# Optimization experiments

Measured on AMD Instinct MI355X. Metric: run time of the kernel, lower is better.

## Reference

```python
import jax, jax.numpy as jnp
import numpy as np

EMBED = 1024
HEADS = 16
HEAD_DIM = EMBED // HEADS
SCALE = HEAD_DIM ** -0.5


def setup_inputs() -> dict:
    key = jax.random.key(0)
    ks = jax.random.split(key, 5)
    B, N = 2, 2048
    x = jax.random.normal(ks[0], (B, N, EMBED), dtype=jnp.float32)
    # qkv Linear: weight [3*EMBED, EMBED], bias [3*EMBED]
    w_qkv = jax.random.normal(ks[1], (3 * EMBED, EMBED), dtype=jnp.float32) * (EMBED ** -0.5)
    b_qkv = jnp.zeros((3 * EMBED,), dtype=jnp.float32)
    # proj Linear: weight [EMBED, EMBED], bias [EMBED]
    w_proj = jax.random.normal(ks[2], (EMBED, EMBED), dtype=jnp.float32) * (EMBED ** -0.5)
    b_proj = jnp.zeros((EMBED,), dtype=jnp.float32)
    return {"x": x, "w_qkv": w_qkv, "b_qkv": b_qkv, "w_proj": w_proj, "b_proj": b_proj}


def reference(x, w_qkv, b_qkv, w_proj, b_proj):
    B, N, _ = x.shape
    # QKV projection: [B, N, 3*EMBED]
    qkv = jnp.einsum('bnc,dc->bnd', x, w_qkv) + b_qkv
    qkv = qkv.reshape(B, N, 3, HEADS, HEAD_DIM).transpose(2, 0, 3, 1, 4)  # [3, B, H, N, Dh]
    q, k, v = qkv[0], qkv[1], qkv[2]
    # Explicit attention: matmul -> scale -> softmax -> matmul (eval mode, no dropout)
    attn = jnp.einsum('bhqd,bhkd->bhqk', q, k) * SCALE
    attn = jax.nn.softmax(attn, axis=-1)
    out = jnp.einsum('bhqk,bhkd->bhqd', attn, v)
    out = out.transpose(0, 2, 1, 3).reshape(B, N, EMBED)
    # Output projection (gamma1 is Identity; dropouts are zero in eval)
    out = jnp.einsum('bnc,dc->bnd', out, w_proj) + b_proj
    return out
```

## Files before the change

kernel.cpp:

```cpp
#include <hip/hip_runtime.h>
#include <stdint.h>

#define SEQ 2048

typedef __attribute__((ext_vector_type(8))) short bf16x8;
typedef __attribute__((ext_vector_type(4))) float f32x4;
typedef __attribute__((ext_vector_type(4))) int i32x4;

typedef const __attribute__((address_space(1))) unsigned int GVT;
typedef __attribute__((address_space(3))) unsigned int LVT;

static __device__ __forceinline__ unsigned short f2bf(float f) {
  unsigned u = __builtin_bit_cast(unsigned, f);
  u += 0x7fffu + ((u >> 16) & 1u);
  return (unsigned short)(u >> 16);
}

static __device__ __forceinline__ unsigned pk_bf16(float lo, float hi) {
  unsigned r;
  asm("v_cvt_pk_bf16_f32 %0, %1, %2" : "=v"(r) : "v"(lo), "v"(hi));
  return r;
}

__global__ __launch_bounds__(256) void cvt3_kernel(
    const float* __restrict__ s0, unsigned short* __restrict__ d0, int n0,
    const float* __restrict__ s1, unsigned short* __restrict__ d1, int n1,
    const float* __restrict__ s2, unsigned short* __restrict__ d2, int n2) {
  int i = blockIdx.x * 256 + threadIdx.x;
  const int stride = gridDim.x * 256;
  const int total = n0 + n1 + n2;
  for (; i < total; i += stride) {
    const float* s;
    unsigned short* d;
    int k;
    if (i < n0) { s = s0; d = d0; k = i; }
    else if (i < n0 + n1) { s = s1; d = d1; k = i - n0; }
    else { s = s2; d = d2; k = i - n0 - n1; }
    float4 v = reinterpret_cast<const float4*>(s)[k];
    ushort4 o;
    o.x = f2bf(v.x); o.y = f2bf(v.y); o.z = f2bf(v.z); o.w = f2bf(v.w);
    reinterpret_cast<ushort4*>(d)[k] = o;
  }
}

__global__ __launch_bounds__(256, 3) void gemm_qkv_kernel(
    const unsigned short* __restrict__ A,
    const unsigned short* __restrict__ Bt,
    const float* __restrict__ bias,
    unsigned short* __restrict__ qb,
    unsigned short* __restrict__ kbuf,
    unsigned short* __restrict__ vtbuf) {
  __shared__ __align__(16) unsigned short As[2][128 * 32];
  __shared__ __align__(16) unsigned short Bs[2][128 * 32];
  const int tid = threadIdx.x;
  const int lane = tid & 63;
  const int wid = tid >> 6;
  const int wr = wid >> 1, wc = wid & 1;
  const int lin = blockIdx.y * 24 + blockIdx.x;
  const int wg = (lin & 7) * 96 + (lin >> 3);
  const int bm = wg / 24, bn = wg % 24;
  const int lr = lane & 15, hg = lane >> 4;

  f32x4 acc[4][4] = {};

  const int r0 = tid >> 2;
  const int c0 = (tid & 3) * 8;

  auto STAGE = [&](int b, int kt) {
    const unsigned short* ga0 = A + (size_t)(bm * 128 + r0) * 1024 + kt * 32 + c0;
    const unsigned short* ga1 = A + (size_t)(bm * 128 + r0 + 64) * 1024 + kt * 32 + c0;
    const unsigned short* gb0 = Bt + (size_t)(bn * 128 + r0) * 1024 + kt * 32 + c0;
    const unsigned short* gb1 = Bt + (size_t)(bn * 128 + r0 + 64) * 1024 + kt * 32 + c0;
    __builtin_amdgcn_global_load_lds((GVT*)ga0, (LVT*)&As[b][tid * 8], 16, 0, 0);
    __builtin_amdgcn_global_load_lds((GVT*)ga1, (LVT*)&As[b][(tid + 256) * 8], 16, 0, 0);
    __builtin_amdgcn_global_load_lds((GVT*)gb0, (LVT*)&Bs[b][tid * 8], 16, 0, 0);
    __builtin_amdgcn_global_load_lds((GVT*)gb1, (LVT*)&Bs[b][(tid + 256) * 8], 16, 0, 0);
  };

  STAGE(0, 0);
  int cur = 0;
  for (int kt = 0; kt < 32; ++kt) {
    __syncthreads();
    if (kt + 1 < 32) STAGE(cur ^ 1, kt + 1);
    bf16x8 af[4], bfr[4];
#pragma unroll
    for (int i = 0; i < 4; ++i) {
      af[i] = *reinterpret_cast<const bf16x8*>(&As[cur][(wr * 64 + i * 16 + lr) * 32 + hg * 8]);
      bfr[i] = *reinterpret_cast<const bf16x8*>(&Bs[cur][(wc * 64 + i * 16 + lr) * 32 + hg * 8]);
    }
    __builtin_amdgcn_s_setprio(1);
#pragma unroll
    for (int i = 0; i < 4; ++i)
#pragma unroll
      for (int j = 0; j < 4; ++j)
        acc[i][j] = __builtin_amdgcn_mfma_f32_16x16x32_bf16(af[i], bfr[j], acc[i][j], 0, 0, 0);
    __builtin_amdgcn_s_setprio(0);
    cur ^= 1;
  }

#pragma unroll
  for (int j = 0; j < 4; ++j) {
    const int col = bn * 128 + wc * 64 + j * 16 + lr;
    const float bv = bias[col];
    const int which = col >> 10;
    const int hh = (col >> 6) & 15;
    const int dh = col & 63;
    const float scl = which == 0 ? 0.18033688011112042f : 1.0f;
#pragma unroll
    for (int i = 0; i < 4; ++i) {
      if (which == 2) {
        const int row0 = bm * 128 + wr * 64 + i * 16 + hg * 4;
        const int b = row0 >> 11, n0 = row0 & 2047;
        ushort4 vv;
        vv.x = f2bf(acc[i][j][0] + bv);
        vv.y = f2bf(acc[i][j][1] + bv);
        vv.z = f2bf(acc[i][j][2] + bv);
        vv.w = f2bf(acc[i][j][3] + bv);
        *reinterpret_cast<ushort4*>(
            &vtbuf[((size_t)((b * 16 + hh) * 64 + dh)) * 2048 + n0]) = vv;
      } else {
        unsigned short* dst = which == 0 ? qb : kbuf;
#pragma unroll
        for (int r = 0; r < 4; ++r) {
          const int row = bm * 128 + wr * 64 + i * 16 + hg * 4 + r;
          const int b = row >> 11, n = row & 2047;
          dst[((size_t)((b * 16 + hh) * 2048 + n)) * 64 + dh] = f2bf((acc[i][j][r] + bv) * scl);
        }
      }
    }
  }
}

__global__ __launch_bounds__(256, 2) void gemm_proj_kernel(
    const unsigned short* __restrict__ A,
    const unsigned short* __restrict__ Bt,
    const float* __restrict__ bias,
    float* __restrict__ out) {
  __shared__ __align__(16) unsigned short As[2][64 * 32];
  __shared__ __align__(16) unsigned short Bs[2][128 * 32];
  const int tid = threadIdx.x;
  const int lane = tid & 63;
  const int wc = tid >> 6;
  const int lin = blockIdx.y * 8 + blockIdx.x;
  const int wg = (lin & 7) * 64 + (lin >> 3);
  const int bm = wg >> 3, bn = wg & 7;
  const int lr = lane & 15, hg = lane >> 4;

  f32x4 acc[4][2] = {};
  const int r0 = tid >> 2;
  const int c0 = (tid & 3) * 8;

  auto STAGE = [&](int b, int kt) {
    const unsigned short* ga0 = A + (size_t)(bm * 64 + r0) * 1024 + kt * 32 + c0;
    const unsigned short* gb0 = Bt + (size_t)(bn * 128 + r0) * 1024 + kt * 32 + c0;
    const unsigned short* gb1 = Bt + (size_t)(bn * 128 + r0 + 64) * 1024 + kt * 32 + c0;
    __builtin_amdgcn_global_load_lds((GVT*)ga0, (LVT*)&As[b][tid * 8], 16, 0, 0);
    __builtin_amdgcn_global_load_lds((GVT*)gb0, (LVT*)&Bs[b][tid * 8], 16, 0, 0);
    __builtin_amdgcn_global_load_lds((GVT*)gb1, (LVT*)&Bs[b][(tid + 256) * 8], 16, 0, 0);
  };

  STAGE(0, 0);
  int cur = 0;
  for (int kt = 0; kt < 32; ++kt) {
    __syncthreads();
    if (kt + 1 < 32) STAGE(cur ^ 1, kt + 1);
    bf16x8 af[4], bfr[2];
#pragma unroll
    for (int i = 0; i < 4; ++i)
      af[i] = *reinterpret_cast<const bf16x8*>(&As[cur][(i * 16 + lr) * 32 + hg * 8]);
#pragma unroll
    for (int j = 0; j < 2; ++j)
      bfr[j] = *reinterpret_cast<const bf16x8*>(&Bs[cur][(wc * 32 + j * 16 + lr) * 32 + hg * 8]);
    __builtin_amdgcn_s_setprio(1);
#pragma unroll
    for (int i = 0; i < 4; ++i)
#pragma unroll
      for (int j = 0; j < 2; ++j)
        acc[i][j] = __builtin_amdgcn_mfma_f32_16x16x32_bf16(af[i], bfr[j], acc[i][j], 0, 0, 0);
    __builtin_amdgcn_s_setprio(0);
    cur ^= 1;
  }

#pragma unroll
  for (int j = 0; j < 2; ++j) {
    const int col = bn * 128 + wc * 32 + j * 16 + lr;
    const float bv = bias[col];
#pragma unroll
    for (int i = 0; i < 4; ++i)
#pragma unroll
      for (int r = 0; r < 4; ++r) {
        const int row = bm * 64 + i * 16 + hg * 4 + r;
        out[(size_t)row * 1024 + col] = acc[i][j][r] + bv;
      }
  }
}

__global__ __launch_bounds__(512, 4) void attn_kernel(
    const unsigned short* __restrict__ qb,
    const unsigned short* __restrict__ kbuf,
    const unsigned short* __restrict__ vt,
    unsigned short* __restrict__ ao) {
  __shared__ __align__(16) unsigned short KVbuf[2][2][2][4096];
  const int tid = threadIdx.x;
  const int lane = tid & 63;
  const int wid = tid >> 6;
  const int ws = wid >> 2;
  const int wq = wid & 3;
  const int lr = lane & 15;
  const int hg = lane >> 4;
  const int lin = blockIdx.y * 16 + blockIdx.x;
  const int wg = (lin & 7) * 64 + (lin >> 3);
  const int qt = wg & 15;
  const int bh = wg >> 4;
  const size_t hbase = (size_t)bh * SEQ * 64;

  bf16x8 qf[2][2];
#pragma unroll
  for (int m = 0; m < 2; ++m) {
    const unsigned short* qp =
        qb + hbase + (size_t)(qt * 128 + wq * 32 + m * 16 + lr) * 64 + hg * 8;
    qf[m][0] = *reinterpret_cast<const bf16x8*>(qp);
    qf[m][1] = *reinterpret_cast<const bf16x8*>(qp + 32);
  }

  f32x4 accO[2][4] = {};
  float l_run[2] = {0.0f, 0.0f};

  const int srow = tid >> 3;
  const int ssw = ((tid & 7) ^ (srow & 7)) * 8;
  auto STAGE = [&](int b, int kt) {
#pragma unroll
    for (int s = 0; s < 2; ++s) {
      const unsigned short* gk =
          kbuf + hbase + (size_t)(s * 1024 + kt * 64 + srow) * 64 + ssw;
      __builtin_amdgcn_global_load_lds((GVT*)gk, (LVT*)&KVbuf[0][s][b][tid * 8], 16, 0, 0);
      const unsigned short* gv =
          vt + hbase + (size_t)srow * 2048 + s * 1024 + kt * 64 + ssw;
      __builtin_amdgcn_global_load_lds((GVT*)gv, (LVT*)&KVbuf[1][s][b][tid * 8], 16, 0, 0);
    }
  };

  STAGE(0, 0);
  int cur = 0;
  const int sw0 = (hg ^ (lr & 7)) * 8;
  const int sw1 = ((hg + 4) ^ (lr & 7)) * 8;

  for (int kt = 0; kt < 16; ++kt) {
    __syncthreads();
    if (kt + 1 < 16) STAGE(cur ^ 1, kt + 1);

    const unsigned short* Ksb = &KVbuf[0][ws][cur][0];
    const unsigned short* Vsb = &KVbuf[1][ws][cur][0];

    f32x4 accT[2][4] = {};
    __builtin_amdgcn_s_setprio(1);
#pragma unroll
    for (int j = 0; j < 4; ++j) {
      const bf16x8 kf0 = *reinterpret_cast<const bf16x8*>(&Ksb[(j * 16 + lr) * 64 + sw0]);
      const bf16x8 kf1 = *reinterpret_cast<const bf16x8*>(&Ksb[(j * 16 + lr) * 64 + sw1]);
      accT[0][j] = __builtin_amdgcn_mfma_f32_16x16x32_bf16(kf0, qf[0][0], accT[0][j], 0, 0, 0);
      accT[0][j] = __builtin_amdgcn_mfma_f32_16x16x32_bf16(kf1, qf[0][1], accT[0][j], 0, 0, 0);
      accT[1][j] = __builtin_amdgcn_mfma_f32_16x16x32_bf16(kf0, qf[1][0], accT[1][j], 0, 0, 0);
      accT[1][j] = __builtin_amdgcn_mfma_f32_16x16x32_bf16(kf1, qf[1][1], accT[1][j], 0, 0, 0);
    }
    __builtin_amdgcn_s_setprio(0);

    bf16x8 pB[2][2];
#pragma unroll
    for (int m = 0; m < 2; ++m) {
      unsigned w[4][2];
      float ps0 = 0.f, ps1 = 0.f;
#pragma unroll
      for (int j = 0; j < 4; ++j) {
        const float p0 = __builtin_amdgcn_exp2f(accT[m][j][0]);
        const float p1 = __builtin_amdgcn_exp2f(accT[m][j][1]);
        const float p2 = __builtin_amdgcn_exp2f(accT[m][j][2]);
        const float p3 = __builtin_amdgcn_exp2f(accT[m][j][3]);
        ps0 += (p0 + p1);
        ps1 += (p2 + p3);
        w[j][0] = pk_bf16(p0, p1);
        w[j][1] = pk_bf16(p2, p3);
      }
      l_run[m] += ps0 + ps1;
#pragma unroll
      for (int h = 0; h < 2; ++h) {
        unsigned e0 = w[2 * h][0], e1 = w[2 * h][1];
        unsigned f0 = w[2 * h + 1][0], f1 = w[2 * h + 1][1];
        asm("v_permlane32_swap_b32 %0, %1" : "+v"(e0), "+v"(f0));
        asm("v_permlane32_swap_b32 %0, %1" : "+v"(e1), "+v"(f1));
        asm("v_permlane16_swap_b32 %0, %1" : "+v"(e0), "+v"(f0));
        asm("v_permlane16_swap_b32 %0, %1" : "+v"(e1), "+v"(f1));
        const i32x4 pw = {(int)e0, (int)e1, (int)f0, (int)f1};
        pB[m][h] = __builtin_bit_cast(bf16x8, pw);
      }
    }

    __builtin_amdgcn_s_setprio(1);
#pragma unroll
    for (int jd = 0; jd < 4; ++jd) {
      const bf16x8 v0 = *reinterpret_cast<const bf16x8*>(&Vsb[(jd * 16 + lr) * 64 + sw0]);
      const bf16x8 v1 = *reinterpret_cast<const bf16x8*>(&Vsb[(jd * 16 + lr) * 64 + sw1]);
      accO[0][jd] = __builtin_amdgcn_mfma_f32_16x16x32_bf16(v0, pB[0][0], accO[0][jd], 0, 0, 0);
      accO[0][jd] = __builtin_amdgcn_mfma_f32_16x16x32_bf16(v1, pB[0][1], accO[0][jd], 0, 0, 0);
      accO[1][jd] = __builtin_amdgcn_mfma_f32_16x16x32_bf16(v0, pB[1][0], accO[1][jd], 0, 0, 0);
      accO[1][jd] = __builtin_amdgcn_mfma_f32_16x16x32_bf16(v1, pB[1][1], accO[1][jd], 0, 0, 0);
    }
    __builtin_amdgcn_s_setprio(0);
    cur ^= 1;
  }

#pragma unroll
  for (int m = 0; m < 2; ++m) {
    l_run[m] += __shfl_xor(l_run[m], 16);
    l_run[m] += __shfl_xor(l_run[m], 32);
  }

  float* scr = (float*)&KVbuf[0][0][0][0];
  const int sbase = (wq * 64 + lane) * 37;
  __syncthreads();
  if (ws == 1) {
#pragma unroll
    for (int m = 0; m < 2; ++m) {
#pragma unroll
      for (int jd = 0; jd < 4; ++jd)
#pragma unroll
        for (int r = 0; r < 4; ++r) scr[sbase + m * 16 + jd * 4 + r] = accO[m][jd][r];
      scr[sbase + 32 + m] = l_run[m];
    }
  }
  __syncthreads();
  if (ws == 0) {
    const int b = bh >> 4, hh = bh & 15;
#pragma unroll
    for (int m = 0; m < 2; ++m) {
      const float inv = 1.0f / (l_run[m] + scr[sbase + 32 + m]);
      const int qrow = qt * 128 + wq * 32 + m * 16 + lr;
      unsigned short* dst = ao + (size_t)(b * 2048 + qrow) * 1024 + hh * 64;
#pragma unroll
      for (int jd = 0; jd < 4; ++jd) {
        const float o0 = (accO[m][jd][0] + scr[sbase + m * 16 + jd * 4 + 0]) * inv;
        const float o1 = (accO[m][jd][1] + scr[sbase + m * 16 + jd * 4 + 1]) * inv;
        const float o2 = (accO[m][jd][2] + scr[sbase + m * 16 + jd * 4 + 2]) * inv;
        const float o3 = (accO[m][jd][3] + scr[sbase + m * 16 + jd * 4 + 3]) * inv;
        uint2 o;
        o.x = pk_bf16(o0, o1);
        o.y = pk_bf16(o2, o3);
        *reinterpret_cast<uint2*>(dst + jd * 16 + hg * 4) = o;
      }
    }
  }
}

extern "C" void kernel_launch(void* const* d_in, const int* in_sizes, int n_in,
                              void* d_out, int out_size, void* d_ws, size_t ws_size,
                              hipStream_t stream) {
  const float* x = (const float*)d_in[0];
  const float* w_qkv = (const float*)d_in[1];
  const float* b_qkv = (const float*)d_in[2];
  const float* w_proj = (const float*)d_in[3];
  const float* b_proj = (const float*)d_in[4];
  float* out = (float*)d_out;
  char* ws = (char*)d_ws;
  unsigned short* x_bf = (unsigned short*)(ws);
  unsigned short* ao_bf = (unsigned short*)(ws);
  unsigned short* wq_bf = (unsigned short*)(ws + (8ull << 20));
  unsigned short* wp_bf = (unsigned short*)(ws + (14ull << 20));
  unsigned short* q_bf = (unsigned short*)(ws + (16ull << 20));
  unsigned short* k_bf = (unsigned short*)(ws + (24ull << 20));
  unsigned short* vt_bf = (unsigned short*)(ws + (32ull << 20));

  cvt3_kernel<<<2048, 256, 0, stream>>>(x, x_bf, 4096 * 1024 / 4,
                                        w_qkv, wq_bf, 3072 * 1024 / 4,
                                        w_proj, wp_bf, 1024 * 1024 / 4);
  gemm_qkv_kernel<<<dim3(24, 32), 256, 0, stream>>>(x_bf, wq_bf, b_qkv, q_bf, k_bf, vt_bf);
  attn_kernel<<<dim3(16, 32), 512, 0, stream>>>(q_bf, k_bf, vt_bf, ao_bf);
  gemm_proj_kernel<<<dim3(8, 64), 256, 0, stream>>>(ao_bf, wp_bf, b_proj, out);
}
```

Before: 112.2 us.

## Stagger softmax-PV across wave groups with triple-buffered V tiles

Wave group 1 now runs its softmax and PV step one tile behind its QK^T step, while group 0 keeps the original order. The two groups therefore run different phases at the same time, interleaving MFMA and exp/VALU work on the CU. V moves to a 3-slot LDS ring so the lagging group can still read its previous tile, which adds shared memory. accT now lives across loop iterations, raising register pressure against the (512,4) launch bounds.

```diff
diff --git a/kernel.cpp b/kernel.cpp
--- a/kernel.cpp
+++ b/kernel.cpp
@@ -200,7 +200,7 @@
     const unsigned short* __restrict__ kbuf,
     const unsigned short* __restrict__ vt,
     unsigned short* __restrict__ ao) {
-  __shared__ __align__(16) unsigned short KVbuf[2][2][2][4096];
+  __shared__ __align__(16) unsigned short SMEM[16384 + 24576];
   const int tid = threadIdx.x;
   const int lane = tid & 63;
   const int wid = tid >> 6;
@@ -225,46 +225,46 @@
 
   f32x4 accO[2][4] = {};
   float l_run[2] = {0.0f, 0.0f};
+  f32x4 accT[2][4];
 
   const int srow = tid >> 3;
   const int ssw = ((tid & 7) ^ (srow & 7)) * 8;
-  auto STAGE = [&](int b, int kt) {
+  auto STAGE = [&](int kt) {
 #pragma unroll
     for (int s = 0; s < 2; ++s) {
       const unsigned short* gk =
           kbuf + hbase + (size_t)(s * 1024 + kt * 64 + srow) * 64 + ssw;
-      __builtin_amdgcn_global_load_lds((GVT*)gk, (LVT*)&KVbuf[0][s][b][tid * 8], 16, 0, 0);
+      __builtin_amdgcn_global_load_lds(
+          (GVT*)gk, (LVT*)&SMEM[(s * 2 + (kt & 1)) * 4096 + tid * 8], 16, 0, 0);
       const unsigned short* gv =
           vt + hbase + (size_t)srow * 2048 + s * 1024 + kt * 64 + ssw;
-      __builtin_amdgcn_global_load_lds((GVT*)gv, (LVT*)&KVbuf[1][s][b][tid * 8], 16, 0, 0);
-    }
-  };
-
-  STAGE(0, 0);
-  int cur = 0;
+      __builtin_amdgcn_global_load_lds(
+          (GVT*)gv, (LVT*)&SMEM[16384 + (s * 3 + (kt % 3)) * 4096 + tid * 8], 16, 0, 0);
+    }
+  };
+
   const int sw0 = (hg ^ (lr & 7)) * 8;
   const int sw1 = ((hg + 4) ^ (lr & 7)) * 8;
 
-  for (int kt = 0; kt < 16; ++kt) {
-    __syncthreads();
-    if (kt + 1 < 16) STAGE(cur ^ 1, kt + 1);
-
-    const unsigned short* Ksb = &KVbuf[0][ws][cur][0];
-    const unsigned short* Vsb = &KVbuf[1][ws][cur][0];
-
-    f32x4 accT[2][4] = {};
+  auto QKT = [&](int kt) {
+    const unsigned short* Ksb = &SMEM[(ws * 2 + (kt & 1)) * 4096];
     __builtin_amdgcn_s_setprio(1);
 #pragma unroll
     for (int j = 0; j < 4; ++j) {
       const bf16x8 kf0 = *reinterpret_cast<const bf16x8*>(&Ksb[(j * 16 + lr) * 64 + sw0]);
       const bf16x8 kf1 = *reinterpret_cast<const bf16x8*>(&Ksb[(j * 16 + lr) * 64 + sw1]);
-      accT[0][j] = __builtin_amdgcn_mfma_f32_16x16x32_bf16(kf0, qf[0][0], accT[0][j], 0, 0, 0);
-      accT[0][j] = __builtin_amdgcn_mfma_f32_16x16x32_bf16(kf1, qf[0][1], accT[0][j], 0, 0, 0);
-      accT[1][j] = __builtin_amdgcn_mfma_f32_16x16x32_bf16(kf0, qf[1][0], accT[1][j], 0, 0, 0);
-      accT[1][j] = __builtin_amdgcn_mfma_f32_16x16x32_bf16(kf1, qf[1][1], accT[1][j], 0, 0, 0);
+      f32x4 z0 = {};
+      z0 = __builtin_amdgcn_mfma_f32_16x16x32_bf16(kf0, qf[0][0], z0, 0, 0, 0);
+      accT[0][j] = __builtin_amdgcn_mfma_f32_16x16x32_bf16(kf1, qf[0][1], z0, 0, 0, 0);
+      f32x4 z1 = {};
+      z1 = __builtin_amdgcn_mfma_f32_16x16x32_bf16(kf0, qf[1][0], z1, 0, 0, 0);
+      accT[1][j] = __builtin_amdgcn_mfma_f32_16x16x32_bf16(kf1, qf[1][1], z1, 0, 0, 0);
     }
     __builtin_amdgcn_s_setprio(0);
-
+  };
+
+  auto SMPV = [&](int vb) {
+    const unsigned short* Vsb = &SMEM[16384 + (ws * 3 + vb) * 4096];
     bf16x8 pB[2][2];
 #pragma unroll
     for (int m = 0; m < 2; ++m) {
@@ -294,7 +294,6 @@
         pB[m][h] = __builtin_bit_cast(bf16x8, pw);
       }
     }
-
     __builtin_amdgcn_s_setprio(1);
 #pragma unroll
     for (int jd = 0; jd < 4; ++jd) {
@@ -306,8 +305,21 @@
       accO[1][jd] = __builtin_amdgcn_mfma_f32_16x16x32_bf16(v1, pB[1][1], accO[1][jd], 0, 0, 0);
     }
     __builtin_amdgcn_s_setprio(0);
-    cur ^= 1;
-  }
+  };
+
+  STAGE(0);
+  for (int kt = 0; kt < 16; ++kt) {
+    __syncthreads();
+    if (kt + 1 < 16) STAGE(kt + 1);
+    if (ws == 0) {
+      QKT(kt);
+      SMPV(kt % 3);
+    } else {
+      if (kt > 0) SMPV((kt - 1) % 3);
+      QKT(kt);
+    }
+  }
+  if (ws == 1) SMPV(15 % 3);
 
 #pragma unroll
   for (int m = 0; m < 2; ++m) {
@@ -315,7 +327,7 @@
     l_run[m] += __shfl_xor(l_run[m], 32);
   }
 
-  float* scr = (float*)&KVbuf[0][0][0][0];
+  float* scr = (float*)&SMEM[0];
   const int sbase = (wq * 64 + lane) * 37;
   __syncthreads();
   if (ws == 1) {
```

Measured after the change: 121.0 us. +7.9%, slower.
